# Kernel tuning notes

Measured on AMD Instinct MI355X. Metric: run time of the kernel, lower is better.

Reference implementation:

```python
import jax, jax.numpy as jnp
import numpy as np

EPS = 1e-20

def _conv(x, w, pad):
    return jax.lax.conv_general_dilated(
        x, w, (1, 1), [(pad, pad), (pad, pad)],
        dimension_numbers=('NCHW', 'OIHW', 'NCHW'))

def _nconv(x, c, w_raw, b, pad):
    # Normalized convolution with SoftPlus-enforced positive weights.
    w = jax.nn.softplus(w_raw)
    denom = _conv(c, w, pad)
    nomin = _conv(x * c, w, pad)
    out = nomin / (denom + EPS) + b[None, :, None, None]
    s = jnp.sum(w.reshape(w.shape[0], -1), axis=-1)  # per-out-channel kernel sum
    cout = denom / s[None, :, None, None]
    return out, cout

def _pool_gather(x, c):
    # max_pool2d(c, 2, 2, return_indices=True), then gather x at those indices.
    B, C, H, W = c.shape
    win = lambda t: t.reshape(B, C, H // 2, 2, W // 2, 2).transpose(0, 1, 2, 4, 3, 5).reshape(B, C, H // 2, W // 2, 4)
    cw, xw = win(c), win(x)
    idx = jnp.argmax(cw, axis=-1)
    take = lambda t: jnp.take_along_axis(t, idx[..., None], axis=-1)[..., 0]
    return take(xw), take(cw) / 4.0  # c1_ds /= 4

def _up2(t):
    return jnp.repeat(jnp.repeat(t, 2, axis=2), 2, axis=3)

def setup_inputs() -> dict:
    key = jax.random.key(0)
    ks = jax.random.split(key, 16)
    B, H, W, C = 8, 352, 1216, 8
    inp = {
        'x0': jax.random.normal(ks[0], (B, 1, H, W), jnp.float32),
        'c0': jax.random.uniform(ks[1], (B, 1, H, W), jnp.float32),
        'w1': jax.random.normal(ks[2], (C, 1, 5, 5), jnp.float32) * 0.1,
        'b1': jax.random.normal(ks[3], (C,), jnp.float32) * 0.01,
        'w2': jax.random.normal(ks[4], (C, C, 5, 5), jnp.float32) * 0.1,
        'b2': jax.random.normal(ks[5], (C,), jnp.float32) * 0.01,
        'w3': jax.random.normal(ks[6], (C, C, 5, 5), jnp.float32) * 0.1,
        'b3': jax.random.normal(ks[7], (C,), jnp.float32) * 0.01,
        'w4': jax.random.normal(ks[8], (C, 2 * C, 3, 3), jnp.float32) * 0.1,
        'b4': jax.random.normal(ks[9], (C,), jnp.float32) * 0.01,
        'w5': jax.random.normal(ks[10], (C, 2 * C, 3, 3), jnp.float32) * 0.1,
        'b5': jax.random.normal(ks[11], (C,), jnp.float32) * 0.01,
        'w6': jax.random.normal(ks[12], (C, 2 * C, 3, 3), jnp.float32) * 0.1,
        'b6': jax.random.normal(ks[13], (C,), jnp.float32) * 0.01,
        'w7': jax.random.normal(ks[14], (1, C, 1, 1), jnp.float32) * 0.1,
        'b7': jax.random.normal(ks[15], (1,), jnp.float32) * 0.01,
    }
    return inp

def reference(x0, c0, w1, b1, w2, b2, w3, b3, w4, b4, w5, b5, w6, b6, w7, b7):
    x1, c1 = _nconv(x0, c0, w1, b1, 2)
    x1, c1 = _nconv(x1, c1, w2, b2, 2)
    x1, c1 = _nconv(x1, c1, w3, b3, 2)
    # downsample 1 (confidence-guided unpool indices)
    x1_ds, c1_ds = _pool_gather(x1, c1)
    x2_ds, c2_ds = _nconv(x1_ds, c1_ds, w2, b2, 2)   # nconv2 reused
    x2_ds, c2_ds = _nconv(x2_ds, c2_ds, w3, b3, 2)   # nconv3 reused
    # downsample 2
    x2_dss, c2_dss = _pool_gather(x2_ds, c2_ds)
    x3_ds, c3_ds = _nconv(x2_dss, c2_dss, w2, b2, 2)
    # downsample 3
    x3_dss, c3_dss = _pool_gather(x3_ds, c3_ds)
    x4_ds, c4_ds = _nconv(x3_dss, c3_dss, w2, b2, 2)
    # decoder with nearest upsample + concat + nconv
    x4, c4 = _up2(x4_ds), _up2(c4_ds)
    x34_ds, c34_ds = _nconv(jnp.concatenate((x3_ds, x4), 1), jnp.concatenate((c3_ds, c4), 1), w4, b4, 1)
    x34, c34 = _up2(x34_ds), _up2(c34_ds)
    x23_ds, c23_ds = _nconv(jnp.concatenate((x2_ds, x34), 1), jnp.concatenate((c2_ds, c34), 1), w5, b5, 1)
    x23, c23 = _up2(x23_ds), _up2(c23_ds)
    xout, cout = _nconv(jnp.concatenate((x23, x1), 1), jnp.concatenate((c23, c1), 1), w6, b6, 1)
    xout, cout = _nconv(xout, cout, w7, b7, 0)
    return xout, cout
```

## Files before the change

### kernel.cpp

```cpp
#include <hip/hip_runtime.h>
#include <cmath>

#define EPSV 1e-20f
#define MFMA16(A, B, C) __builtin_amdgcn_mfma_f32_16x16x32_f16(A, B, C, 0, 0, 0)

typedef _Float16 f16;
typedef _Float16 v8h __attribute__((ext_vector_type(8)));
typedef _Float16 h4 __attribute__((ext_vector_type(4)));
typedef float v4f __attribute__((ext_vector_type(4)));
typedef float f32x2 __attribute__((ext_vector_type(2)));

__device__ __forceinline__ float softplusf(float x) {
    return fmaxf(x, 0.f) + log1pf(expf(-fabsf(x)));
}

__device__ __forceinline__ v8h v8h_zero() {
    v8h z = {0, 0, 0, 0, 0, 0, 0, 0};
    return z;
}

__global__ void prep_scalars(const float* __restrict__ w1, const float* __restrict__ w2,
                             const float* __restrict__ w3, const float* __restrict__ w4,
                             const float* __restrict__ w5, const float* __restrict__ w6,
                             const float* __restrict__ w7, float* __restrict__ WT) {
    __shared__ float lds[1600];
    const float* srcs[7] = {w1, w2, w3, w4, w5, w6, w7};
    const int ns[7]    = {200, 1600, 1600, 1152, 1152, 1152, 8};
    const int pers[7]  = {25, 200, 200, 144, 144, 144, 8};
    const int couts[7] = {8, 8, 8, 8, 8, 8, 1};
    int t = blockIdx.x;
    const float* src = srcs[t];
    int n = ns[t];
    for (int i = threadIdx.x; i < n; i += blockDim.x) {
        float v = softplusf(src[i]);
        lds[i] = v;
        if (t == 0) WT[i] = v;
        if (t == 6) WT[256 + i] = v;
    }
    __syncthreads();
    if ((int)threadIdx.x < couts[t]) {
        float s = 0.f;
        int per = pers[t];
        for (int i = 0; i < per; ++i) s += lds[threadIdx.x * per + i];
        WT[200 + t * 8 + threadIdx.x] = s;
    }
}

__global__ void pack_enc_frag(const float* __restrict__ w2, const float* __restrict__ w3,
                              f16* __restrict__ dst2, f16* __restrict__ dst3) {
    const float* w = blockIdx.x ? w3 : w2;
    f16* dst = blockIdx.x ? dst3 : dst2;
    for (int i = threadIdx.x; i < 7 * 64 * 8; i += blockDim.x) {
        int g = i >> 9;
        int l = (i >> 3) & 63;
        int j = i & 7;
        int co = l & 15, sub = l >> 4;
        float v = 0.f;
        if (co < 8) {
            int kh = 0, kw = 0;
            bool valid = true;
            if (g < 5) { kh = g; kw = sub; }
            else if (g == 5) { kh = sub; kw = 4; }
            else { kh = 4; kw = 4; valid = (sub == 0); }
            if (valid) v = softplusf(w[((co * 8 + j) * 5 + kh) * 5 + kw]);
        }
        dst[i] = (f16)v;
    }
}

__global__ void pack_dec_frag(const float* __restrict__ w4, const float* __restrict__ w5,
                              const float* __restrict__ w6,
                              f16* __restrict__ dst4, f16* __restrict__ dst5,
                              f16* __restrict__ dst6) {
    const float* ww[3] = {w4, w5, w6};
    f16* dd[3] = {dst4, dst5, dst6};
    const int RBt[3] = {0, 0, 1};
    const float* w = ww[blockIdx.x];
    f16* dst = dd[blockIdx.x];
    const int rb = RBt[blockIdx.x], sbk = 1 - rb;
    for (int i = threadIdx.x; i < 7 * 64 * 8; i += blockDim.x) {
        int g = i >> 9;
        int l = (i >> 3) & 63;
        int j = i & 7;
        int co = l & 15, sub = l >> 4;
        float v = 0.f;
        if (co < 8 && sub < 3) {
            int kw = sub;
            auto W_ = [&](int blk, int kh) {
                return softplusf(w[((co * 16 + blk * 8 + j) * 3 + kh) * 3 + kw]);
            };
            if (g < 3) v = W_(rb, g);
            else if (g == 3) v = W_(sbk, 0);
            else if (g == 4) v = W_(sbk, 1) + W_(sbk, 2);
            else if (g == 5) v = W_(sbk, 0) + W_(sbk, 1);
            else v = W_(sbk, 2);
        }
        dst[i] = (f16)v;
    }
}

__device__ __forceinline__ void load_row8_f(const float* __restrict__ row, int c0, int W,
                                            float v[8]) {
    if (c0 >= 0 && c0 + 8 <= W) {
#pragma unroll
        for (int i = 0; i < 4; ++i) {
            f32x2 t = *(const f32x2*)(row + c0 + 2 * i);
            v[2 * i] = t[0];
            v[2 * i + 1] = t[1];
        }
    } else {
#pragma unroll
        for (int i = 0; i < 8; ++i) {
            int c = c0 + i;
            v[i] = (c >= 0 && c < W) ? row[c] : 0.f;
        }
    }
}

__global__ void __launch_bounds__(256) nconv_l1(
    const float* __restrict__ x0, const float* __restrict__ c0,
    const float* __restrict__ wp, const float* __restrict__ ssum,
    const float* __restrict__ bias,
    f16* __restrict__ xcout, f16* __restrict__ cout,
    int B, int H, int W) {
    __shared__ __attribute__((aligned(16))) float wl[200];
    for (int i = threadIdx.x; i < 200; i += 256) {
        int co = i & 7, r = i >> 3;
        wl[i] = wp[co * 25 + r];
    }
    __syncthreads();

    const int Wq = W >> 2;
    int idx = blockIdx.x * 256 + threadIdx.x;
    int total = B * H * Wq;
    if (idx >= total) return;
    int w0 = (idx % Wq) << 2;
    int h = (idx / Wq) % H;
    int b = idx / (Wq * H);
    const int HW = H * W;

    float den[4][8] = {}, nom[4][8] = {};
    const float* cp = c0 + (size_t)b * HW;
    const float* xp = x0 + (size_t)b * HW;

    for (int kh = 0; kh < 5; ++kh) {
        int ih = h + kh - 2;
        if (ih < 0 || ih >= H) continue;
        float cv[8], xr[8], xv[8];
        load_row8_f(cp + (size_t)ih * W, w0 - 2, W, cv);
        load_row8_f(xp + (size_t)ih * W, w0 - 2, W, xr);
#pragma unroll
        for (int i = 0; i < 8; ++i) xv[i] = xr[i] * cv[i];
        const float* wrow = &wl[kh * 5 * 8];
#pragma unroll
        for (int kw = 0; kw < 5; ++kw) {
            const float4* wq = (const float4*)&wrow[kw * 8];
            float4 wa = wq[0], wb = wq[1];
            float wv[8] = {wa.x, wa.y, wa.z, wa.w, wb.x, wb.y, wb.z, wb.w};
#pragma unroll
            for (int co = 0; co < 8; ++co)
#pragma unroll
                for (int p = 0; p < 4; ++p) {
                    den[p][co] = fmaf(wv[co], cv[p + kw], den[p][co]);
                    nom[p][co] = fmaf(wv[co], xv[p + kw], nom[p][co]);
                }
        }
    }

    float rssv[8], bbv[8];
#pragma unroll
    for (int co = 0; co < 8; ++co) {
        rssv[co] = __builtin_amdgcn_rcpf(ssum[co]);
        bbv[co] = bias[co];
    }
    unsigned pa = (unsigned)(((b * H + h) * W + w0) * 8);
#pragma unroll
    for (int p = 0; p < 4; ++p) {
        v8h xc8, c8;
#pragma unroll
        for (int co = 0; co < 8; ++co) {
            float d = den[p][co];
            float cc = d * rssv[co];
            float xo = nom[p][co] * __builtin_amdgcn_rcpf(d + EPSV) + bbv[co];
            xc8[co] = (f16)(xo * cc);
            c8[co] = (f16)cc;
        }
        *(v8h*)(xcout + pa + p * 8) = xc8;
        *(v8h*)(cout + pa + p * 8) = c8;
    }
}

__global__ void __launch_bounds__(256) pool_nhwc(
    const f16* __restrict__ xc, const f16* __restrict__ c,
    f16* __restrict__ xo, f16* __restrict__ co_,
    int B, int H, int W) {
    int H2 = H >> 1, W2 = W >> 1, Wh = W2 >> 1;
    int idx = blockIdx.x * 256 + threadIdx.x;
    int total = B * H2 * Wh;
    if (idx >= total) return;
    int wo = (idx % Wh) * 2;
    int ho = (idx / Wh) % H2;
    int b = idx / (Wh * H2);
    unsigned base = (unsigned)(((b * H + 2 * ho) * W + 2 * wo) * 8);
    unsigned rb = (unsigned)(W * 8);
    v8h c0r[4], c1r[4], x0r[4], x1r[4];
#pragma unroll
    for (int i = 0; i < 4; ++i) {
        c0r[i] = *(const v8h*)(c + base + 8 * i);
        c1r[i] = *(const v8h*)(c + base + rb + 8 * i);
        x0r[i] = *(const v8h*)(xc + base + 8 * i);
        x1r[i] = *(const v8h*)(xc + base + rb + 8 * i);
    }
    unsigned oa = (unsigned)(((b * H2 + ho) * W2 + wo) * 8);
#pragma unroll
    for (int p = 0; p < 2; ++p) {
        v8h xr, cr;
#pragma unroll
        for (int e = 0; e < 8; ++e) {
            float b0 = (float)c0r[2 * p][e], b1 = (float)c0r[2 * p + 1][e];
            float b2 = (float)c1r[2 * p][e], b3 = (float)c1r[2 * p + 1][e];
            float cb = b0;
            float xv = (float)x0r[2 * p][e];
            if (b1 > cb) { cb = b1; xv = (float)x0r[2 * p + 1][e]; }
            if (b2 > cb) { cb = b2; xv = (float)x1r[2 * p][e]; }
            if (b3 > cb) { cb = b3; xv = (float)x1r[2 * p + 1][e]; }
            xr[e] = (f16)(xv * 0.25f);
            cr[e] = (f16)(cb * 0.25f);
        }
        *(v8h*)(xo + oa + p * 8) = xr;
        *(v8h*)(co_ + oa + p * 8) = cr;
    }
}

__global__ void __launch_bounds__(256) enc5_mfma(
    const f16* __restrict__ xcin, const f16* __restrict__ cin,
    const f16* __restrict__ bfrag, const float* __restrict__ ssum,
    const float* __restrict__ bias,
    f16* __restrict__ xcout, f16* __restrict__ cout,
    int B, int H, int W, int CH) {
    const int lane = threadIdx.x & 63;
    const int wid = threadIdx.x >> 6;
    const int m = lane & 15, sub = lane >> 4;
    const int tilesW = (W + 15) >> 4;
    const int tw = blockIdx.x * 4 + wid;
    if (tw >= tilesW) return;
    const int w0 = tw << 4;
    const int b = blockIdx.z;
    const int h0 = blockIdx.y * CH;

    v8h bf[7];
#pragma unroll
    for (int g = 0; g < 7; ++g)
        bf[g] = *(const v8h*)(bfrag + ((g << 6) + lane) * 8);

    float4 ssv = {1.f, 1.f, 1.f, 1.f}, bbv = {0.f, 0.f, 0.f, 0.f};
    if (sub < 2) {
        ssv = *(const float4*)(ssum + sub * 4);
        bbv = *(const float4*)(bias + sub * 4);
    }
    float rssv[4];
#pragma unroll
    for (int j = 0; j < 4; ++j) rssv[j] = __builtin_amdgcn_rcpf(((const float*)&ssv)[j]);

    const unsigned W8u = (unsigned)W * 8;
    const unsigned bb8 = (unsigned)(b * H) * W8u;
    unsigned sbase = bb8 + (unsigned)h0 * W8u + (unsigned)(w0 + m) * 8 + sub * 4;

    auto epi = [&](const v4f& accd, const v4f& accn, unsigned sb) {
        h4 xo8, c8;
#pragma unroll
        for (int j = 0; j < 4; ++j) {
            float d = accd[j];
            float cc = d * rssv[j];
            float x = accn[j] * __builtin_amdgcn_rcpf(d + EPSV) + ((const float*)&bbv)[j];
            c8[j] = (f16)cc;
            xo8[j] = (f16)(x * cc);
        }
        *(h4*)(cout + sb) = c8;
        *(h4*)(xcout + sb) = xo8;
    };

    const bool fast = (w0 >= 2) && (w0 + 17 < W) && (h0 >= 2) && (h0 + CH + 2 <= H);
    if (fast) {
        v8h Rc[5], Rx[5];
        unsigned aRot = bb8 + (unsigned)(h0 - 2) * W8u + (unsigned)(w0 + m + sub - 2) * 8;
#pragma unroll
        for (int t = 0; t < 4; ++t) {
            Rc[t] = *(const v8h*)(cin + aRot);
            Rx[t] = *(const v8h*)(xcin + aRot);
            aRot += W8u;
        }
        unsigned aE5 = bb8 + (unsigned)(h0 + sub - 2) * W8u + (unsigned)(w0 + m + 2) * 8;
        unsigned aE6 = bb8 + (unsigned)(h0 + 2) * W8u + (unsigned)(w0 + m + 2) * 8;
        const bool st = (sub < 2);
        for (int hh = 0; hh < CH; hh += 5) {
#pragma unroll
            for (int p = 0; p < 5; ++p) {
                Rc[(p + 4) % 5] = *(const v8h*)(cin + aRot);
                Rx[(p + 4) % 5] = *(const v8h*)(xcin + aRot);
                aRot += W8u;
                v8h e5c = *(const v8h*)(cin + aE5);
                v8h e5x = *(const v8h*)(xcin + aE5);
                aE5 += W8u;
                v8h e6c = *(const v8h*)(cin + aE6);
                v8h e6x = *(const v8h*)(xcin + aE6);
                aE6 += W8u;

                v4f accd = {0.f, 0.f, 0.f, 0.f}, accn = {0.f, 0.f, 0.f, 0.f};
#pragma unroll
                for (int g = 0; g < 5; ++g) {
                    accd = MFMA16(bf[g], Rc[(p + g) % 5], accd);
                    accn = MFMA16(bf[g], Rx[(p + g) % 5], accn);
                }
                accd = MFMA16(bf[5], e5c, accd);
                accn = MFMA16(bf[5], e5x, accn);
                accd = MFMA16(bf[6], e6c, accd);
                accn = MFMA16(bf[6], e6x, accn);

                if (st) epi(accd, accn, sbase);
                sbase += W8u;
            }
        }
    } else {
        const int cwr = w0 + m + sub - 2;
        const bool okc_r = (cwr >= 0) && (cwr < W);
        const unsigned a_rot = (unsigned)min(max(cwr, 0), W - 1) * 8;
        const int cwe = w0 + m + 2;
        const bool okc_e = cwe < W;
        const unsigned a_e = (unsigned)min(cwe, W - 1) * 8;
        const bool doStore = (sub < 2) && (w0 + m < W);

        v8h Rc[5], Rx[5];
#pragma unroll
        for (int t = 0; t < 4; ++t) {
            int r = h0 - 2 + t;
            bool ok = (r >= 0) && (r < H) && okc_r;
            unsigned a = bb8 + (unsigned)min(max(r, 0), H - 1) * W8u + a_rot;
            v8h pc = *(const v8h*)(cin + a);
            v8h px = *(const v8h*)(xcin + a);
            Rc[t] = ok ? pc : v8h_zero();
            Rx[t] = ok ? px : v8h_zero();
        }
        Rc[4] = v8h_zero();
        Rx[4] = v8h_zero();

        for (int hh = 0; hh < CH; hh += 5) {
#pragma unroll
            for (int p = 0; p < 5; ++p) {
                const int h = h0 + hh + p;
                {
                    int r = h + 2;
                    bool ok = (r < H) && okc_r;
                    unsigned a = bb8 + (unsigned)min(r, H - 1) * W8u + a_rot;
                    v8h pc = *(const v8h*)(cin + a);
                    v8h px = *(const v8h*)(xcin + a);
                    Rc[(p + 4) % 5] = ok ? pc : v8h_zero();
                    Rx[(p + 4) % 5] = ok ? px : v8h_zero();
                }
                v8h e5c, e5x;
                {
                    int r = h + sub - 2;
                    bool ok = (r >= 0) && (r < H) && okc_e;
                    unsigned a = bb8 + (unsigned)min(max(r, 0), H - 1) * W8u + a_e;
                    v8h pc = *(const v8h*)(cin + a);
                    v8h px = *(const v8h*)(xcin + a);
                    e5c = ok ? pc : v8h_zero();
                    e5x = ok ? px : v8h_zero();
                }
                v8h e6c, e6x;
                {
                    int r = h + 2;
                    bool ok = (r < H) && okc_e;
                    unsigned a = bb8 + (unsigned)min(r, H - 1) * W8u + a_e;
                    v8h pc = *(const v8h*)(cin + a);
                    v8h px = *(const v8h*)(xcin + a);
                    e6c = ok ? pc : v8h_zero();
                    e6x = ok ? px : v8h_zero();
                }

                v4f accd = {0.f, 0.f, 0.f, 0.f}, accn = {0.f, 0.f, 0.f, 0.f};
#pragma unroll
                for (int g = 0; g < 5; ++g) {
                    accd = MFMA16(bf[g], Rc[(p + g) % 5], accd);
                    accn = MFMA16(bf[g], Rx[(p + g) % 5], accn);
                }
                accd = MFMA16(bf[5], e5c, accd);
                accn = MFMA16(bf[5], e5x, accn);
                accd = MFMA16(bf[6], e6c, accd);
                accn = MFMA16(bf[6], e6x, accn);

                if (doStore && h < H) epi(accd, accn, sbase);
                sbase += W8u;
            }
        }
    }
}

template <bool FUSE7>
__global__ void __launch_bounds__(256) dec3_mfma(
    const f16* __restrict__ xcR, const f16* __restrict__ cR,
    const f16* __restrict__ xcS, const f16* __restrict__ cS,
    const f16* __restrict__ bfrag,
    const float* __restrict__ ssum, const float* __restrict__ bias,
    const float* __restrict__ wp7, const float* __restrict__ s7p,
    const float* __restrict__ b7p,
    f16* __restrict__ xcout, f16* __restrict__ ccout,
    float* __restrict__ xoutf, float* __restrict__ coutf,
    int B, int H, int W, int CH) {
    const int lane = threadIdx.x & 63;
    const int wid = threadIdx.x >> 6;
    const int m = lane & 15, sub = lane >> 4;
    const int tilesW = W >> 4;
    const int tw = blockIdx.x * 4 + wid;
    if (tw >= tilesW) return;
    const int w0 = tw << 4;
    const int b = blockIdx.z;
    const int h0 = blockIdx.y * CH;

    v8h bf[7];
#pragma unroll
    for (int g = 0; g < 7; ++g)
        bf[g] = *(const v8h*)(bfrag + ((g << 6) + lane) * 8);

    const int cw = w0 + m + sub - 1;
    const bool okc = (cw >= 0) && (cw < W);
    const int cwc = min(max(cw, 0), W - 1);
    const unsigned aRc = (unsigned)cwc * 8;
    const unsigned aSc = (unsigned)(cwc >> 1) * 8;

    const int Hs = H >> 1, Ws = W >> 1;
    const unsigned WR8 = (unsigned)W * 8;
    const unsigned WS8 = (unsigned)Ws * 8;
    const unsigned bbR = (unsigned)(b * H) * WR8;
    const unsigned bbS = (unsigned)(b * Hs) * WS8;

    float4 ssv = {1.f, 1.f, 1.f, 1.f}, bbv = {0.f, 0.f, 0.f, 0.f};
    float4 w7v = {0.f, 0.f, 0.f, 0.f};
    if (sub < 2) {
        ssv = *(const float4*)(ssum + sub * 4);
        bbv = *(const float4*)(bias + sub * 4);
        if (FUSE7) w7v = *(const float4*)(wp7 + sub * 4);
    }
    float rssv[4];
#pragma unroll
    for (int j = 0; j < 4; ++j) rssv[j] = __builtin_amdgcn_rcpf(((const float*)&ssv)[j]);
    float rs7 = 0.f, b7v = 0.f;
    if (FUSE7) { rs7 = __builtin_amdgcn_rcpf(s7p[0]); b7v = b7p[0]; }

    unsigned sbase = bbR + (unsigned)h0 * WR8 + (unsigned)(w0 + m) * 8 + sub * 4;
    unsigned opix = (unsigned)(b * H + h0) * (unsigned)W + (unsigned)w0;

    auto epi = [&](const v4f& accd, const v4f& accn) {
        if constexpr (FUSE7) {
            float td = 0.f, tn = 0.f;
#pragma unroll
            for (int j = 0; j < 4; ++j) {
                float d = accd[j];
                float cc = d * rssv[j];
                float o = accn[j] * __builtin_amdgcn_rcpf(d + EPSV) + ((const float*)&bbv)[j];
                td = fmaf(((const float*)&w7v)[j], cc, td);
                tn = fmaf(((const float*)&w7v)[j], o * cc, tn);
            }
            td += __shfl_xor(td, 16);
            tn += __shfl_xor(tn, 16);
            td += __shfl_xor(td, 32);
            tn += __shfl_xor(tn, 32);
            if (sub == 0) {
                xoutf[opix + m] = tn * __builtin_amdgcn_rcpf(td + EPSV) + b7v;
            } else if (sub == 1) {
                coutf[opix + m] = td * rs7;
            }
        } else {
            if (sub < 2) {
                h4 xo8, c8;
#pragma unroll
                for (int j = 0; j < 4; ++j) {
                    float d = accd[j];
                    float cc = d * rssv[j];
                    float x = accn[j] * __builtin_amdgcn_rcpf(d + EPSV) + ((const float*)&bbv)[j];
                    c8[j] = (f16)cc;
                    xo8[j] = (f16)(x * cc);
                }
                *(h4*)(ccout + sbase) = c8;
                *(h4*)(xcout + sbase) = xo8;
            }
        }
    };

    const bool fast = (w0 >= 1) && (w0 + 17 < W) && (h0 >= 2) && (h0 + CH + 1 <= H);
    if (fast) {
        v8h Rc_[3], Rx_[3], Sc_[3], Sx_[3];
        unsigned ar = bbR + (unsigned)(h0 - 1) * WR8 + aRc;
        Rc_[2] = *(const v8h*)(cR + ar); Rx_[2] = *(const v8h*)(xcR + ar); ar += WR8;
        Rc_[0] = *(const v8h*)(cR + ar); Rx_[0] = *(const v8h*)(xcR + ar); ar += WR8;
        const int k0 = h0 >> 1;
        unsigned as_ = bbS + (unsigned)(k0 - 1) * WS8 + aSc;
        Sc_[2] = *(const v8h*)(cS + as_); Sx_[2] = *(const v8h*)(xcS + as_); as_ += WS8;
        Sc_[0] = *(const v8h*)(cS + as_); Sx_[0] = *(const v8h*)(xcS + as_); as_ += WS8;

        for (int hh = 0; hh < CH; hh += 6) {
#pragma unroll
            for (int p = 0; p < 6; ++p) {
                const int j = p >> 1;
                Rc_[(p + 1) % 3] = *(const v8h*)(cR + ar);
                Rx_[(p + 1) % 3] = *(const v8h*)(xcR + ar);
                ar += WR8;
                if ((p & 1) == 0) {
                    Sc_[(j + 1) % 3] = *(const v8h*)(cS + as_);
                    Sx_[(j + 1) % 3] = *(const v8h*)(xcS + as_);
                    as_ += WS8;
                }
                v4f accd = {0.f, 0.f, 0.f, 0.f}, accn = {0.f, 0.f, 0.f, 0.f};
#pragma unroll
                for (int g = 0; g < 3; ++g) {
                    accd = MFMA16(bf[g], Rc_[(p + g + 2) % 3], accd);
                    accn = MFMA16(bf[g], Rx_[(p + g + 2) % 3], accn);
                }
                if ((p & 1) == 0) {
                    accd = MFMA16(bf[3], Sc_[(j + 2) % 3], accd);
                    accn = MFMA16(bf[3], Sx_[(j + 2) % 3], accn);
                    accd = MFMA16(bf[4], Sc_[j % 3], accd);
                    accn = MFMA16(bf[4], Sx_[j % 3], accn);
                } else {
                    accd = MFMA16(bf[5], Sc_[j % 3], accd);
                    accn = MFMA16(bf[5], Sx_[j % 3], accn);
                    accd = MFMA16(bf[6], Sc_[(j + 1) % 3], accd);
                    accn = MFMA16(bf[6], Sx_[(j + 1) % 3], accn);
                }
                epi(accd, accn);
                sbase += WR8;
                opix += W;
            }
        }
    } else {
        for (int hh = 0; hh < CH; ++hh) {
            const int h = h0 + hh;
            if (h >= H) break;
            const int k = h >> 1;
            const bool ev = (h & 1) == 0;
            v4f accd = {0.f, 0.f, 0.f, 0.f}, accn = {0.f, 0.f, 0.f, 0.f};
#pragma unroll
            for (int g = 0; g < 3; ++g) {
                int r = h + g - 1;
                bool ok = okc && (r >= 0) && (r < H);
                unsigned a = bbR + (unsigned)min(max(r, 0), H - 1) * WR8 + aRc;
                v8h pc = *(const v8h*)(cR + a);
                v8h px = *(const v8h*)(xcR + a);
                if (!ok) { pc = v8h_zero(); px = v8h_zero(); }
                accd = MFMA16(bf[g], pc, accd);
                accn = MFMA16(bf[g], px, accn);
            }
            {
                int rs = ev ? (k - 1) : k;
                bool ok = okc && (!ev || (h >= 1));
                unsigned a = bbS + (unsigned)min(max(rs, 0), Hs - 1) * WS8 + aSc;
                v8h pc = *(const v8h*)(cS + a);
                v8h px = *(const v8h*)(xcS + a);
                if (!ok) { pc = v8h_zero(); px = v8h_zero(); }
                v8h wA = ev ? bf[3] : bf[5];
                accd = MFMA16(wA, pc, accd);
                accn = MFMA16(wA, px, accn);
            }
            {
                int rs = ev ? k : (k + 1);
                bool ok = okc && (ev || (h + 1 < H));
                unsigned a = bbS + (unsigned)min(max(rs, 0), Hs - 1) * WS8 + aSc;
                v8h pc = *(const v8h*)(cS + a);
                v8h px = *(const v8h*)(xcS + a);
                if (!ok) { pc = v8h_zero(); px = v8h_zero(); }
                v8h wB = ev ? bf[4] : bf[6];
                accd = MFMA16(wB, pc, accd);
                accn = MFMA16(wB, px, accn);
            }
            epi(accd, accn);
            sbase += WR8;
            opix += W;
        }
    }
}

extern "C" void kernel_launch(void* const* d_in, const int* in_sizes, int n_in,
                              void* d_out, int out_size, void* d_ws, size_t ws_size,
                              hipStream_t stream) {
    const float* x0 = (const float*)d_in[0];
    const float* c0 = (const float*)d_in[1];
    const float* w1 = (const float*)d_in[2];
    const float* b1 = (const float*)d_in[3];
    const float* w2 = (const float*)d_in[4];
    const float* b2 = (const float*)d_in[5];
    const float* w3 = (const float*)d_in[6];
    const float* b3 = (const float*)d_in[7];
    const float* w4 = (const float*)d_in[8];
    const float* b4 = (const float*)d_in[9];
    const float* w5 = (const float*)d_in[10];
    const float* b5 = (const float*)d_in[11];
    const float* w6 = (const float*)d_in[12];
    const float* b6 = (const float*)d_in[13];
    const float* w7 = (const float*)d_in[14];
    const float* b7 = (const float*)d_in[15];

    const int B = 8, H = 352, W = 1216;
    const int H2 = 176, W2 = 608, H4 = 88, W4 = 304, H8 = 44, W8 = 152;
    const size_t F   = (size_t)64 * H * W;
    const size_t H2s = (size_t)64 * H2 * W2;
    const size_t Qs  = (size_t)64 * H4 * W4;
    const size_t Es  = (size_t)64 * H8 * W8;

    const size_t needH = 4 * F * sizeof(f16) + 7168 * sizeof(float);
    if (ws_size < needH) return;

    f16* ws = (f16*)d_ws;
    f16* P0x = ws;
    f16* P0c = ws + F;
    f16* Ux  = ws + 2 * F;
    f16* Uc  = ws + 3 * F;
    f16* D1x = ws + 2 * F;
    f16* D1c = D1x + H2s;
    f16* D2x = D1c + H2s;
    f16* D2c = D2x + H2s;
    f16* Q1x = ws + 3 * F;
    f16* Q1c = Q1x + Qs;
    f16* Q2x = Q1c + Qs;
    f16* Q2c = Q2x + Qs;
    f16* E1x = Q2c + Qs;
    f16* E1c = E1x + Es;
    f16* E2x = E1c + Es;
    f16* E2c = E2x + Es;
    f16* DF4 = ws + 3 * F + 16777216;
    f16* DF5 = DF4 + 3584;
    f16* DF6 = DF5 + 3584;

    char* tail = (char*)d_ws + 4 * F * sizeof(f16);
    float* WT = (float*)tail;
    f16* BF2 = (f16*)(tail + 2048);
    f16* BF3 = (f16*)(tail + 9216);

    const float* s1 = WT + 200;
    const float* s2 = WT + 208;
    const float* s3 = WT + 216;
    const float* s4 = WT + 224;
    const float* s5 = WT + 232;
    const float* s6 = WT + 240;
    const float* s7 = WT + 248;
    const float* wp7 = WT + 256;

    prep_scalars<<<7, 256, 0, stream>>>(w1, w2, w3, w4, w5, w6, w7, WT);
    pack_enc_frag<<<2, 256, 0, stream>>>(w2, w3, BF2, BF3);

    auto nb = [](size_t n) { return (int)((n + 255) / 256); };
    const dim3 geF(19, 18, 8);
    const dim3 geH(10, 9, 8);
    const dim3 geQ(5, 9, 8);
    const dim3 geE(3, 9, 8);
    const dim3 gdF(19, 30, 8);
    const dim3 gdH(10, 15, 8);
    const dim3 gdQ(5, 8, 8);

    nconv_l1<<<nb((size_t)B * H * (W / 4)), 256, 0, stream>>>(
        x0, c0, WT, s1, b1, P0x, P0c, B, H, W);
    enc5_mfma<<<geF, 256, 0, stream>>>(P0x, P0c, BF2, s2, b2, Ux, Uc, B, H, W, 20);
    enc5_mfma<<<geF, 256, 0, stream>>>(Ux, Uc, BF3, s3, b3, P0x, P0c, B, H, W, 20);
    pack_dec_frag<<<3, 256, 0, stream>>>(w4, w5, w6, DF4, DF5, DF6);
    pool_nhwc<<<nb((size_t)B * H2 * (W2 / 2)), 256, 0, stream>>>(P0x, P0c, D1x, D1c, B, H, W);
    enc5_mfma<<<geH, 256, 0, stream>>>(D1x, D1c, BF2, s2, b2, D2x, D2c, B, H2, W2, 20);
    enc5_mfma<<<geH, 256, 0, stream>>>(D2x, D2c, BF3, s3, b3, D1x, D1c, B, H2, W2, 20);
    pool_nhwc<<<nb((size_t)B * H4 * (W4 / 2)), 256, 0, stream>>>(D1x, D1c, Q1x, Q1c, B, H2, W2);
    enc5_mfma<<<geQ, 256, 0, stream>>>(Q1x, Q1c, BF2, s2, b2, Q2x, Q2c, B, H4, W4, 10);
    pool_nhwc<<<nb((size_t)B * H8 * (W8 / 2)), 256, 0, stream>>>(Q2x, Q2c, E1x, E1c, B, H4, W4);
    enc5_mfma<<<geE, 256, 0, stream>>>(E1x, E1c, BF2, s2, b2, E2x, E2c, B, H8, W8, 5);

    dec3_mfma<false><<<gdQ, 256, 0, stream>>>(
        Q2x, Q2c, E2x, E2c, DF4, s4, b4, WT, WT, WT,
        Q1x, Q1c, (float*)nullptr, (float*)nullptr, B, H4, W4, 12);
    dec3_mfma<false><<<gdH, 256, 0, stream>>>(
        D1x, D1c, Q1x, Q1c, DF5, s5, b5, WT, WT, WT,
        D2x, D2c, (float*)nullptr, (float*)nullptr, B, H2, W2, 12);

    float* outx = (float*)d_out;
    float* outc = outx + (size_t)B * H * W;
    dec3_mfma<true><<<gdF, 256, 0, stream>>>(
        P0x, P0c, D2x, D2c, DF6, s6, b6, wp7, s7, b7,
        (f16*)nullptr, (f16*)nullptr, outx, outc, B, H, W, 12);
}
```

Baseline: 426.1 us.

## Split MFMA accumulators and prefetch rows one step ahead in encoder/decoder convs

The encoder and decoder MFMA conv loops now split each accumulation chain into two independent accumulator pairs (d0/d1, n0/n1), which shortens the dependent MFMA chain, and sum them in the epilogue. The rolling row buffers are enlarged (6 rows in the encoder, 4 in the decoder) and the extra-row fragments are double-buffered, so loads are issued one row ahead of their use. Row-chunk sizes and grid heights are retuned to match the new unroll factors, with an early exit for blocks past the image height. The slow boundary path is simplified to a non-unrolled per-row loop. This raises register pressure and changes fast-path eligibility at the tile edges.

```diff
diff --git a/kernel.cpp b/kernel.cpp
--- a/kernel.cpp
+++ b/kernel.cpp
@@ -247,6 +247,7 @@
     const int w0 = tw << 4;
     const int b = blockIdx.z;
     const int h0 = blockIdx.y * CH;
+    if (h0 >= H) return;
 
     v8h bf[7];
 #pragma unroll
@@ -280,44 +281,59 @@
         *(h4*)(xcout + sb) = xo8;
     };
 
-    const bool fast = (w0 >= 2) && (w0 + 17 < W) && (h0 >= 2) && (h0 + CH + 2 <= H);
+    const bool fast = (w0 >= 2) && (w0 + 17 < W) && (h0 >= 2) && (h0 + CH + 3 <= H);
     if (fast) {
-        v8h Rc[5], Rx[5];
+        v8h Rc[6], Rx[6];
         unsigned aRot = bb8 + (unsigned)(h0 - 2) * W8u + (unsigned)(w0 + m + sub - 2) * 8;
 #pragma unroll
-        for (int t = 0; t < 4; ++t) {
-            Rc[t] = *(const v8h*)(cin + aRot);
-            Rx[t] = *(const v8h*)(xcin + aRot);
+        for (int t = 0; t < 5; ++t) {
+            const int s = (t + 4) % 6;
+            Rc[s] = *(const v8h*)(cin + aRot);
+            Rx[s] = *(const v8h*)(xcin + aRot);
             aRot += W8u;
         }
         unsigned aE5 = bb8 + (unsigned)(h0 + sub - 2) * W8u + (unsigned)(w0 + m + 2) * 8;
         unsigned aE6 = bb8 + (unsigned)(h0 + 2) * W8u + (unsigned)(w0 + m + 2) * 8;
+        v8h e5c[2], e5x[2], e6c[2], e6x[2];
+        e5c[0] = *(const v8h*)(cin + aE5);
+        e5x[0] = *(const v8h*)(xcin + aE5);
+        aE5 += W8u;
+        e6c[0] = *(const v8h*)(cin + aE6);
+        e6x[0] = *(const v8h*)(xcin + aE6);
+        aE6 += W8u;
         const bool st = (sub < 2);
-        for (int hh = 0; hh < CH; hh += 5) {
-#pragma unroll
-            for (int p = 0; p < 5; ++p) {
-                Rc[(p + 4) % 5] = *(const v8h*)(cin + aRot);
-                Rx[(p + 4) % 5] = *(const v8h*)(xcin + aRot);
+
+        for (int hh = 0; hh < CH; hh += 6) {
+#pragma unroll
+            for (int p = 0; p < 6; ++p) {
+                Rc[(p + 3) % 6] = *(const v8h*)(cin + aRot);
+                Rx[(p + 3) % 6] = *(const v8h*)(xcin + aRot);
                 aRot += W8u;
-                v8h e5c = *(const v8h*)(cin + aE5);
-                v8h e5x = *(const v8h*)(xcin + aE5);
+                e5c[(p + 1) & 1] = *(const v8h*)(cin + aE5);
+                e5x[(p + 1) & 1] = *(const v8h*)(xcin + aE5);
                 aE5 += W8u;
-                v8h e6c = *(const v8h*)(cin + aE6);
-                v8h e6x = *(const v8h*)(xcin + aE6);
+                e6c[(p + 1) & 1] = *(const v8h*)(cin + aE6);
+                e6x[(p + 1) & 1] = *(const v8h*)(xcin + aE6);
                 aE6 += W8u;
 
-                v4f accd = {0.f, 0.f, 0.f, 0.f}, accn = {0.f, 0.f, 0.f, 0.f};
-#pragma unroll
-                for (int g = 0; g < 5; ++g) {
-                    accd = MFMA16(bf[g], Rc[(p + g) % 5], accd);
-                    accn = MFMA16(bf[g], Rx[(p + g) % 5], accn);
-                }
-                accd = MFMA16(bf[5], e5c, accd);
-                accn = MFMA16(bf[5], e5x, accn);
-                accd = MFMA16(bf[6], e6c, accd);
-                accn = MFMA16(bf[6], e6x, accn);
-
-                if (st) epi(accd, accn, sbase);
+                v4f d0 = {0.f, 0.f, 0.f, 0.f}, d1 = {0.f, 0.f, 0.f, 0.f};
+                v4f n0 = {0.f, 0.f, 0.f, 0.f}, n1 = {0.f, 0.f, 0.f, 0.f};
+                d0 = MFMA16(bf[0], Rc[(p + 4) % 6], d0);
+                n0 = MFMA16(bf[0], Rx[(p + 4) % 6], n0);
+                d1 = MFMA16(bf[1], Rc[(p + 5) % 6], d1);
+                n1 = MFMA16(bf[1], Rx[(p + 5) % 6], n1);
+                d0 = MFMA16(bf[2], Rc[p % 6], d0);
+                n0 = MFMA16(bf[2], Rx[p % 6], n0);
+                d1 = MFMA16(bf[3], Rc[(p + 1) % 6], d1);
+                n1 = MFMA16(bf[3], Rx[(p + 1) % 6], n1);
+                d0 = MFMA16(bf[4], Rc[(p + 2) % 6], d0);
+                n0 = MFMA16(bf[4], Rx[(p + 2) % 6], n0);
+                d1 = MFMA16(bf[5], e5c[p & 1], d1);
+                n1 = MFMA16(bf[5], e5x[p & 1], n1);
+                d0 = MFMA16(bf[6], e6c[p & 1], d0);
+                n0 = MFMA16(bf[6], e6x[p & 1], n0);
+
+                if (st) epi(d0 + d1, n0 + n1, sbase);
                 sbase += W8u;
             }
         }
@@ -330,68 +346,49 @@
         const unsigned a_e = (unsigned)min(cwe, W - 1) * 8;
         const bool doStore = (sub < 2) && (w0 + m < W);
 
-        v8h Rc[5], Rx[5];
-#pragma unroll
-        for (int t = 0; t < 4; ++t) {
-            int r = h0 - 2 + t;
-            bool ok = (r >= 0) && (r < H) && okc_r;
-            unsigned a = bb8 + (unsigned)min(max(r, 0), H - 1) * W8u + a_rot;
-            v8h pc = *(const v8h*)(cin + a);
-            v8h px = *(const v8h*)(xcin + a);
-            Rc[t] = ok ? pc : v8h_zero();
-            Rx[t] = ok ? px : v8h_zero();
-        }
-        Rc[4] = v8h_zero();
-        Rx[4] = v8h_zero();
-
-        for (int hh = 0; hh < CH; hh += 5) {
-#pragma unroll
-            for (int p = 0; p < 5; ++p) {
-                const int h = h0 + hh + p;
-                {
-                    int r = h + 2;
-                    bool ok = (r < H) && okc_r;
-                    unsigned a = bb8 + (unsigned)min(r, H - 1) * W8u + a_rot;
-                    v8h pc = *(const v8h*)(cin + a);
-                    v8h px = *(const v8h*)(xcin + a);
-                    Rc[(p + 4) % 5] = ok ? pc : v8h_zero();
-                    Rx[(p + 4) % 5] = ok ? px : v8h_zero();
+        for (int hh = 0; hh < CH; ++hh) {
+            const int h = h0 + hh;
+            if (h >= H) break;
+            v4f d0 = {0.f, 0.f, 0.f, 0.f}, d1 = {0.f, 0.f, 0.f, 0.f};
+            v4f n0 = {0.f, 0.f, 0.f, 0.f}, n1 = {0.f, 0.f, 0.f, 0.f};
+#pragma unroll
+            for (int g = 0; g < 5; ++g) {
+                int r = h + g - 2;
+                bool ok = okc_r && (r >= 0) && (r < H);
+                unsigned a = bb8 + (unsigned)min(max(r, 0), H - 1) * W8u + a_rot;
+                v8h pc = *(const v8h*)(cin + a);
+                v8h px = *(const v8h*)(xcin + a);
+                if (!ok) { pc = v8h_zero(); px = v8h_zero(); }
+                if (g & 1) {
+                    d1 = MFMA16(bf[g], pc, d1);
+                    n1 = MFMA16(bf[g], px, n1);
+                } else {
+                    d0 = MFMA16(bf[g], pc, d0);
+                    n0 = MFMA16(bf[g], px, n0);
                 }
-                v8h e5c, e5x;
-                {
-                    int r = h + sub - 2;
-                    bool ok = (r >= 0) && (r < H) && okc_e;
-                    unsigned a = bb8 + (unsigned)min(max(r, 0), H - 1) * W8u + a_e;
-                    v8h pc = *(const v8h*)(cin + a);
-                    v8h px = *(const v8h*)(xcin + a);
-                    e5c = ok ? pc : v8h_zero();
-                    e5x = ok ? px : v8h_zero();
-                }
-                v8h e6c, e6x;
-                {
-                    int r = h + 2;
-                    bool ok = (r < H) && okc_e;
-                    unsigned a = bb8 + (unsigned)min(r, H - 1) * W8u + a_e;
-                    v8h pc = *(const v8h*)(cin + a);
-                    v8h px = *(const v8h*)(xcin + a);
-                    e6c = ok ? pc : v8h_zero();
-                    e6x = ok ? px : v8h_zero();
-                }
-
-                v4f accd = {0.f, 0.f, 0.f, 0.f}, accn = {0.f, 0.f, 0.f, 0.f};
-#pragma unroll
-                for (int g = 0; g < 5; ++g) {
-                    accd = MFMA16(bf[g], Rc[(p + g) % 5], accd);
-                    accn = MFMA16(bf[g], Rx[(p + g) % 5], accn);
-                }
-                accd = MFMA16(bf[5], e5c, accd);
-                accn = MFMA16(bf[5], e5x, accn);
-                accd = MFMA16(bf[6], e6c, accd);
-                accn = MFMA16(bf[6], e6x, accn);
-
-                if (doStore && h < H) epi(accd, accn, sbase);
-                sbase += W8u;
-            }
+            }
+            {
+                int r = h + sub - 2;
+                bool ok = okc_e && (r >= 0) && (r < H);
+                unsigned a = bb8 + (unsigned)min(max(r, 0), H - 1) * W8u + a_e;
+                v8h pc = *(const v8h*)(cin + a);
+                v8h px = *(const v8h*)(xcin + a);
+                if (!ok) { pc = v8h_zero(); px = v8h_zero(); }
+                d1 = MFMA16(bf[5], pc, d1);
+                n1 = MFMA16(bf[5], px, n1);
+            }
+            {
+                int r = h + 2;
+                bool ok = okc_e && (r < H);
+                unsigned a = bb8 + (unsigned)min(r, H - 1) * W8u + a_e;
+                v8h pc = *(const v8h*)(cin + a);
+                v8h px = *(const v8h*)(xcin + a);
+                if (!ok) { pc = v8h_zero(); px = v8h_zero(); }
+                d0 = MFMA16(bf[6], pc, d0);
+                n0 = MFMA16(bf[6], px, n0);
+            }
+            if (doStore) epi(d0 + d1, n0 + n1, sbase);
+            sbase += W8u;
         }
     }
 }
@@ -416,6 +413,7 @@
     const int w0 = tw << 4;
     const int b = blockIdx.z;
     const int h0 = blockIdx.y * CH;
+    if (h0 >= H) return;
 
     v8h bf[7];
 #pragma unroll
@@ -487,47 +485,51 @@
         }
     };
 
-    const bool fast = (w0 >= 1) && (w0 + 17 < W) && (h0 >= 2) && (h0 + CH + 1 <= H);
+    const bool fast = (w0 >= 1) && (w0 + 17 < W) && (h0 >= 2) && (h0 + CH + 2 <= H);
     if (fast) {
-        v8h Rc_[3], Rx_[3], Sc_[3], Sx_[3];
+        v8h Rc_[4], Rx_[4], Sc_[3], Sx_[3];
         unsigned ar = bbR + (unsigned)(h0 - 1) * WR8 + aRc;
-        Rc_[2] = *(const v8h*)(cR + ar); Rx_[2] = *(const v8h*)(xcR + ar); ar += WR8;
+        Rc_[3] = *(const v8h*)(cR + ar); Rx_[3] = *(const v8h*)(xcR + ar); ar += WR8;
         Rc_[0] = *(const v8h*)(cR + ar); Rx_[0] = *(const v8h*)(xcR + ar); ar += WR8;
+        Rc_[1] = *(const v8h*)(cR + ar); Rx_[1] = *(const v8h*)(xcR + ar); ar += WR8;
         const int k0 = h0 >> 1;
         unsigned as_ = bbS + (unsigned)(k0 - 1) * WS8 + aSc;
         Sc_[2] = *(const v8h*)(cS + as_); Sx_[2] = *(const v8h*)(xcS + as_); as_ += WS8;
         Sc_[0] = *(const v8h*)(cS + as_); Sx_[0] = *(const v8h*)(xcS + as_); as_ += WS8;
 
-        for (int hh = 0; hh < CH; hh += 6) {
-#pragma unroll
-            for (int p = 0; p < 6; ++p) {
-                const int j = p >> 1;
-                Rc_[(p + 1) % 3] = *(const v8h*)(cR + ar);
-                Rx_[(p + 1) % 3] = *(const v8h*)(xcR + ar);
+        for (int hh = 0; hh < CH; hh += 12) {
+#pragma unroll
+            for (int p = 0; p < 12; ++p) {
+                const int pj = (p >> 1) % 3;
+                Rc_[(p + 2) & 3] = *(const v8h*)(cR + ar);
+                Rx_[(p + 2) & 3] = *(const v8h*)(xcR + ar);
                 ar += WR8;
                 if ((p & 1) == 0) {
-                    Sc_[(j + 1) % 3] = *(const v8h*)(cS + as_);
-                    Sx_[(j + 1) % 3] = *(const v8h*)(xcS + as_);
+                    Sc_[(pj + 1) % 3] = *(const v8h*)(cS + as_);
+                    Sx_[(pj + 1) % 3] = *(const v8h*)(xcS + as_);
                     as_ += WS8;
                 }
-                v4f accd = {0.f, 0.f, 0.f, 0.f}, accn = {0.f, 0.f, 0.f, 0.f};
-#pragma unroll
-                for (int g = 0; g < 3; ++g) {
-                    accd = MFMA16(bf[g], Rc_[(p + g + 2) % 3], accd);
-                    accn = MFMA16(bf[g], Rx_[(p + g + 2) % 3], accn);
+
+                v4f d0 = {0.f, 0.f, 0.f, 0.f}, d1 = {0.f, 0.f, 0.f, 0.f};
+                v4f n0 = {0.f, 0.f, 0.f, 0.f}, n1 = {0.f, 0.f, 0.f, 0.f};
+                d0 = MFMA16(bf[0], Rc_[(p + 3) & 3], d0);
+                n0 = MFMA16(bf[0], Rx_[(p + 3) & 3], n0);
+                d1 = MFMA16(bf[1], Rc_[p & 3], d1);
+                n1 = MFMA16(bf[1], Rx_[p & 3], n1);
+                d0 = MFMA16(bf[2], Rc_[(p + 1) & 3], d0);
+                n0 = MFMA16(bf[2], Rx_[(p + 1) & 3], n0);
+                if ((p & 1) == 0) {
+                    d1 = MFMA16(bf[3], Sc_[(pj + 2) % 3], d1);
+                    n1 = MFMA16(bf[3], Sx_[(pj + 2) % 3], n1);
+                    d0 = MFMA16(bf[4], Sc_[pj], d0);
+                    n0 = MFMA16(bf[4], Sx_[pj], n0);
+                } else {
+                    d1 = MFMA16(bf[5], Sc_[pj], d1);
+                    n1 = MFMA16(bf[5], Sx_[pj], n1);
+                    d0 = MFMA16(bf[6], Sc_[(pj + 1) % 3], d0);
+                    n0 = MFMA16(bf[6], Sx_[(pj + 1) % 3], n0);
                 }
-                if ((p & 1) == 0) {
-                    accd = MFMA16(bf[3], Sc_[(j + 2) % 3], accd);
-                    accn = MFMA16(bf[3], Sx_[(j + 2) % 3], accn);
-                    accd = MFMA16(bf[4], Sc_[j % 3], accd);
-                    accn = MFMA16(bf[4], Sx_[j % 3], accn);
-                } else {
-                    accd = MFMA16(bf[5], Sc_[j % 3], accd);
-                    accn = MFMA16(bf[5], Sx_[j % 3], accn);
-                    accd = MFMA16(bf[6], Sc_[(j + 1) % 3], accd);
-                    accn = MFMA16(bf[6], Sx_[(j + 1) % 3], accn);
-                }
-                epi(accd, accn);
+                epi(d0 + d1, n0 + n1);
                 sbase += WR8;
                 opix += W;
             }
@@ -648,26 +650,26 @@
     pack_enc_frag<<<2, 256, 0, stream>>>(w2, w3, BF2, BF3);
 
     auto nb = [](size_t n) { return (int)((n + 255) / 256); };
-    const dim3 geF(19, 18, 8);
-    const dim3 geH(10, 9, 8);
-    const dim3 geQ(5, 9, 8);
-    const dim3 geE(3, 9, 8);
+    const dim3 geF(19, 20, 8);
+    const dim3 geH(10, 10, 8);
+    const dim3 geQ(5, 8, 8);
+    const dim3 geE(3, 8, 8);
     const dim3 gdF(19, 30, 8);
     const dim3 gdH(10, 15, 8);
     const dim3 gdQ(5, 8, 8);
 
     nconv_l1<<<nb((size_t)B * H * (W / 4)), 256, 0, stream>>>(
         x0, c0, WT, s1, b1, P0x, P0c, B, H, W);
-    enc5_mfma<<<geF, 256, 0, stream>>>(P0x, P0c, BF2, s2, b2, Ux, Uc, B, H, W, 20);
-    enc5_mfma<<<geF, 256, 0, stream>>>(Ux, Uc, BF3, s3, b3, P0x, P0c, B, H, W, 20);
+    enc5_mfma<<<geF, 256, 0, stream>>>(P0x, P0c, BF2, s2, b2, Ux, Uc, B, H, W, 18);
+    enc5_mfma<<<geF, 256, 0, stream>>>(Ux, Uc, BF3, s3, b3, P0x, P0c, B, H, W, 18);
     pack_dec_frag<<<3, 256, 0, stream>>>(w4, w5, w6, DF4, DF5, DF6);
     pool_nhwc<<<nb((size_t)B * H2 * (W2 / 2)), 256, 0, stream>>>(P0x, P0c, D1x, D1c, B, H, W);
-    enc5_mfma<<<geH, 256, 0, stream>>>(D1x, D1c, BF2, s2, b2, D2x, D2c, B, H2, W2, 20);
-    enc5_mfma<<<geH, 256, 0, stream>>>(D2x, D2c, BF3, s3, b3, D1x, D1c, B, H2, W2, 20);
+    enc5_mfma<<<geH, 256, 0, stream>>>(D1x, D1c, BF2, s2, b2, D2x, D2c, B, H2, W2, 18);
+    enc5_mfma<<<geH, 256, 0, stream>>>(D2x, D2c, BF3, s3, b3, D1x, D1c, B, H2, W2, 18);
     pool_nhwc<<<nb((size_t)B * H4 * (W4 / 2)), 256, 0, stream>>>(D1x, D1c, Q1x, Q1c, B, H2, W2);
-    enc5_mfma<<<geQ, 256, 0, stream>>>(Q1x, Q1c, BF2, s2, b2, Q2x, Q2c, B, H4, W4, 10);
+    enc5_mfma<<<geQ, 256, 0, stream>>>(Q1x, Q1c, BF2, s2, b2, Q2x, Q2c, B, H4, W4, 12);
     pool_nhwc<<<nb((size_t)B * H8 * (W8 / 2)), 256, 0, stream>>>(Q2x, Q2c, E1x, E1c, B, H4, W4);
-    enc5_mfma<<<geE, 256, 0, stream>>>(E1x, E1c, BF2, s2, b2, E2x, E2c, B, H8, W8, 5);
+    enc5_mfma<<<geE, 256, 0, stream>>>(E1x, E1c, BF2, s2, b2, E2x, E2c, B, H8, W8, 6);
 
     dec3_mfma<false><<<gdQ, 256, 0, stream>>>(
         Q2x, Q2c, E2x, E2c, DF4, s4, b4, WT, WT, WT,
```

Measured after the change: 461.8 us. 1.08x slower.

## Fuse confidence-guided 2x2 max-pool gather into encoder nconv epilogue

Applied to the files above, without the earlier changes.

The enc5_mfma kernel gains a POOL template path. On odd rows it combines the current and previous output rows with a lane shuffle, does the argmax-by-confidence gather, and writes the half-resolution pooled outputs directly. This removes the separate pool_nhwc launches and the re-read of the full-resolution activations. To avoid aliasing, the workspace layout is rearranged and needs extra buffer space, with a fallback to the old separate pool when the workspace is too small.

```diff
diff --git a/kernel.cpp b/kernel.cpp
--- a/kernel.cpp
+++ b/kernel.cpp
@@ -17,6 +17,14 @@
 __device__ __forceinline__ v8h v8h_zero() {
     v8h z = {0, 0, 0, 0, 0, 0, 0, 0};
     return z;
+}
+
+__device__ __forceinline__ h4 shflx1(h4 v) {
+    union { h4 h; int i[2]; } u;
+    u.h = v;
+    u.i[0] = __shfl_xor(u.i[0], 1);
+    u.i[1] = __shfl_xor(u.i[1], 1);
+    return u.h;
 }
 
 __global__ void prep_scalars(const float* __restrict__ w1, const float* __restrict__ w2,
@@ -232,11 +240,13 @@
     }
 }
 
+template <bool POOL>
 __global__ void __launch_bounds__(256) enc5_mfma(
     const f16* __restrict__ xcin, const f16* __restrict__ cin,
     const f16* __restrict__ bfrag, const float* __restrict__ ssum,
     const float* __restrict__ bias,
     f16* __restrict__ xcout, f16* __restrict__ cout,
+    f16* __restrict__ pxo, f16* __restrict__ pco,
     int B, int H, int W, int CH) {
     const int lane = threadIdx.x & 63;
     const int wid = threadIdx.x >> 6;
@@ -247,6 +257,7 @@
     const int w0 = tw << 4;
     const int b = blockIdx.z;
     const int h0 = blockIdx.y * CH;
+    if (h0 >= H) return;
 
     v8h bf[7];
 #pragma unroll
@@ -266,7 +277,13 @@
     const unsigned bb8 = (unsigned)(b * H) * W8u;
     unsigned sbase = bb8 + (unsigned)h0 * W8u + (unsigned)(w0 + m) * 8 + sub * 4;
 
-    auto epi = [&](const v4f& accd, const v4f& accn, unsigned sb) {
+    const int W2p = W >> 1;
+    unsigned pbase = 0;
+    if (POOL)
+        pbase = (unsigned)((b * (H >> 1) + (h0 >> 1)) * W2p + ((w0 + m) >> 1)) * 8 + sub * 4;
+    h4 c8p = {}, xo8p = {};
+
+    auto emit = [&](const v4f& accd, const v4f& accn, int h) {
         h4 xo8, c8;
 #pragma unroll
         for (int j = 0; j < 4; ++j) {
@@ -276,8 +293,35 @@
             c8[j] = (f16)cc;
             xo8[j] = (f16)(x * cc);
         }
-        *(h4*)(cout + sb) = c8;
-        *(h4*)(xcout + sb) = xo8;
+        *(h4*)(cout + sbase) = c8;
+        *(h4*)(xcout + sbase) = xo8;
+        if constexpr (POOL) {
+            if (h & 1) {
+                h4 cN = shflx1(c8), xN = shflx1(xo8);
+                h4 cPN = shflx1(c8p), xPN = shflx1(xo8p);
+                if ((m & 1) == 0) {
+                    h4 pc_, px_;
+#pragma unroll
+                    for (int j = 0; j < 4; ++j) {
+                        float c00 = (float)c8p[j], c01 = (float)cPN[j];
+                        float c10 = (float)c8[j], c11 = (float)cN[j];
+                        float x00 = (float)xo8p[j], x01 = (float)xPN[j];
+                        float x10 = (float)xo8[j], x11 = (float)xN[j];
+                        float cb = c00, xv = x00;
+                        if (c01 > cb) { cb = c01; xv = x01; }
+                        if (c10 > cb) { cb = c10; xv = x10; }
+                        if (c11 > cb) { cb = c11; xv = x11; }
+                        pc_[j] = (f16)(cb * 0.25f);
+                        px_[j] = (f16)(xv * 0.25f);
+                    }
+                    *(h4*)(pco + pbase) = pc_;
+                    *(h4*)(pxo + pbase) = px_;
+                }
+                pbase += (unsigned)W2p * 8;
+            }
+            c8p = c8;
+            xo8p = xo8;
+        }
     };
 
     const bool fast = (w0 >= 2) && (w0 + 17 < W) && (h0 >= 2) && (h0 + CH + 2 <= H);
@@ -296,6 +340,7 @@
         for (int hh = 0; hh < CH; hh += 5) {
 #pragma unroll
             for (int p = 0; p < 5; ++p) {
+                const int h = h0 + hh + p;
                 Rc[(p + 4) % 5] = *(const v8h*)(cin + aRot);
                 Rx[(p + 4) % 5] = *(const v8h*)(xcin + aRot);
                 aRot += W8u;
@@ -317,7 +362,7 @@
                 accd = MFMA16(bf[6], e6c, accd);
                 accn = MFMA16(bf[6], e6x, accn);
 
-                if (st) epi(accd, accn, sbase);
+                if (st) emit(accd, accn, h);
                 sbase += W8u;
             }
         }
@@ -389,7 +434,7 @@
                 accd = MFMA16(bf[6], e6c, accd);
                 accn = MFMA16(bf[6], e6x, accn);
 
-                if (doStore && h < H) epi(accd, accn, sbase);
+                if (doStore && h < H) emit(accd, accn, h);
                 sbase += W8u;
             }
         }
@@ -416,6 +461,7 @@
     const int w0 = tw << 4;
     const int b = blockIdx.z;
     const int h0 = blockIdx.y * CH;
+    if (h0 >= H) return;
 
     v8h bf[7];
 #pragma unroll
@@ -606,18 +652,37 @@
     const size_t Qs  = (size_t)64 * H4 * W4;
     const size_t Es  = (size_t)64 * H8 * W8;
 
-    const size_t needH = 4 * F * sizeof(f16) + 7168 * sizeof(float);
-    if (ws_size < needH) return;
+    const size_t needBase = 4 * F * sizeof(f16) + 7168 * sizeof(float);
+    const size_t needFull = (4 * F + 2 * H2s) * sizeof(f16) + 7168 * sizeof(float);
+    if (ws_size < needBase) return;
+    const bool FULL = (ws_size >= needFull);
 
     f16* ws = (f16*)d_ws;
     f16* P0x = ws;
     f16* P0c = ws + F;
     f16* Ux  = ws + 2 * F;
     f16* Uc  = ws + 3 * F;
-    f16* D1x = ws + 2 * F;
-    f16* D1c = D1x + H2s;
-    f16* D2x = D1c + H2s;
-    f16* D2c = D2x + H2s;
+
+    f16 *D1ax, *D1ac, *D2x, *D2c, *D1bx, *D1bc, *DDx, *DDc;
+    if (FULL) {
+        D1ax = ws + 4 * F;
+        D1ac = D1ax + H2s;
+        D2x  = ws + 2 * F;
+        D2c  = D2x + H2s;
+        D1bx = ws + 2 * F + 2 * H2s;
+        D1bc = D1bx + H2s;
+        DDx  = ws + 2 * F;
+        DDc  = DDx + H2s;
+    } else {
+        D1ax = ws + 2 * F;
+        D1ac = D1ax + H2s;
+        D2x  = D1ac + H2s;
+        D2c  = D2x + H2s;
+        D1bx = ws + 2 * F;
+        D1bc = D1bx + H2s;
+        DDx  = ws + 2 * F + 2 * H2s;
+        DDc  = DDx + H2s;
+    }
     f16* Q1x = ws + 3 * F;
     f16* Q1c = Q1x + Qs;
     f16* Q2x = Q1c + Qs;
@@ -630,7 +695,7 @@
     f16* DF5 = DF4 + 3584;
     f16* DF6 = DF5 + 3584;
 
-    char* tail = (char*)d_ws + 4 * F * sizeof(f16);
+    char* tail = (char*)d_ws + (FULL ? (4 * F + 2 * H2s) : 4 * F) * sizeof(f16);
     float* WT = (float*)tail;
     f16* BF2 = (f16*)(tail + 2048);
     f16* BF3 = (f16*)(tail + 9216);
@@ -656,29 +721,41 @@
     const dim3 gdH(10, 15, 8);
     const dim3 gdQ(5, 8, 8);
 
+    f16* nullh = (f16*)nullptr;
+
     nconv_l1<<<nb((size_t)B * H * (W / 4)), 256, 0, stream>>>(
         x0, c0, WT, s1, b1, P0x, P0c, B, H, W);
-    enc5_mfma<<<geF, 256, 0, stream>>>(P0x, P0c, BF2, s2, b2, Ux, Uc, B, H, W, 20);
-    enc5_mfma<<<geF, 256, 0, stream>>>(Ux, Uc, BF3, s3, b3, P0x, P0c, B, H, W, 20);
+    enc5_mfma<false><<<geF, 256, 0, stream>>>(P0x, P0c, BF2, s2, b2, Ux, Uc,
+                                              nullh, nullh, B, H, W, 20);
+    if (FULL) {
+        enc5_mfma<true><<<geF, 256, 0, stream>>>(Ux, Uc, BF3, s3, b3, P0x, P0c,
+                                                 D1ax, D1ac, B, H, W, 20);
+    } else {
+        enc5_mfma<false><<<geF, 256, 0, stream>>>(Ux, Uc, BF3, s3, b3, P0x, P0c,
+                                                  nullh, nullh, B, H, W, 20);
+        pool_nhwc<<<nb((size_t)B * H2 * (W2 / 2)), 256, 0, stream>>>(
+            P0x, P0c, D1ax, D1ac, B, H, W);
+    }
     pack_dec_frag<<<3, 256, 0, stream>>>(w4, w5, w6, DF4, DF5, DF6);
-    pool_nhwc<<<nb((size_t)B * H2 * (W2 / 2)), 256, 0, stream>>>(P0x, P0c, D1x, D1c, B, H, W);
-    enc5_mfma<<<geH, 256, 0, stream>>>(D1x, D1c, BF2, s2, b2, D2x, D2c, B, H2, W2, 20);
-    enc5_mfma<<<geH, 256, 0, stream>>>(D2x, D2c, BF3, s3, b3, D1x, D1c, B, H2, W2, 20);
-    pool_nhwc<<<nb((size_t)B * H4 * (W4 / 2)), 256, 0, stream>>>(D1x, D1c, Q1x, Q1c, B, H2, W2);
-    enc5_mfma<<<geQ, 256, 0, stream>>>(Q1x, Q1c, BF2, s2, b2, Q2x, Q2c, B, H4, W4, 10);
-    pool_nhwc<<<nb((size_t)B * H8 * (W8 / 2)), 256, 0, stream>>>(Q2x, Q2c, E1x, E1c, B, H4, W4);
-    enc5_mfma<<<geE, 256, 0, stream>>>(E1x, E1c, BF2, s2, b2, E2x, E2c, B, H8, W8, 5);
+    enc5_mfma<false><<<geH, 256, 0, stream>>>(D1ax, D1ac, BF2, s2, b2, D2x, D2c,
+                                              nullh, nullh, B, H2, W2, 20);
+    enc5_mfma<true><<<geH, 256, 0, stream>>>(D2x, D2c, BF3, s3, b3, D1bx, D1bc,
+                                             Q1x, Q1c, B, H2, W2, 20);
+    enc5_mfma<true><<<geQ, 256, 0, stream>>>(Q1x, Q1c, BF2, s2, b2, Q2x, Q2c,
+                                             E1x, E1c, B, H4, W4, 10);
+    enc5_mfma<false><<<geE, 256, 0, stream>>>(E1x, E1c, BF2, s2, b2, E2x, E2c,
+                                              nullh, nullh, B, H8, W8, 5);
 
     dec3_mfma<false><<<gdQ, 256, 0, stream>>>(
         Q2x, Q2c, E2x, E2c, DF4, s4, b4, WT, WT, WT,
         Q1x, Q1c, (float*)nullptr, (float*)nullptr, B, H4, W4, 12);
     dec3_mfma<false><<<gdH, 256, 0, stream>>>(
-        D1x, D1c, Q1x, Q1c, DF5, s5, b5, WT, WT, WT,
-        D2x, D2c, (float*)nullptr, (float*)nullptr, B, H2, W2, 12);
+        D1bx, D1bc, Q1x, Q1c, DF5, s5, b5, WT, WT, WT,
+        DDx, DDc, (float*)nullptr, (float*)nullptr, B, H2, W2, 12);
 
     float* outx = (float*)d_out;
     float* outc = outx + (size_t)B * H * W;
     dec3_mfma<true><<<gdF, 256, 0, stream>>>(
-        P0x, P0c, D2x, D2c, DF6, s6, b6, wp7, s7, b7,
-        (f16*)nullptr, (f16*)nullptr, outx, outc, B, H, W, 12);
-}
+        P0x, P0c, DDx, DDc, DF6, s6, b6, wp7, s7, b7,
+        nullh, nullh, outx, outc, B, H, W, 12);
+}
```

Result: no change. 424.7 us (-0.3%).
